# Kernel tuning notes

Hardware: AMD Instinct MI355X
Metric: run time of the kernel (lower is better)

Reference implementation:

```python
import jax, jax.numpy as jnp
import numpy as np

WS = 7   # window size
SS = 3   # shift size


def _ln(x, g, b):
    m = x.mean(-1, keepdims=True)
    v = ((x - m) ** 2).mean(-1, keepdims=True)
    return (x - m) / jnp.sqrt(v + 1e-5) * g + b


def setup_inputs() -> dict:
    key = jax.random.key(0)
    ks = jax.random.split(key, 8)
    B, H, W, C, nh = 64, 56, 56, 96, 3
    N = WS * WS
    x = jax.random.normal(ks[0], (B, H * W, C), jnp.float32)

    # Swin SW-MSA attention mask: [nW, N, N], 0 where attention is allowed, -100 otherwise
    img = np.zeros((H, W), np.int32)
    cnt = 0
    for hs in (slice(0, H - WS), slice(H - WS, H - SS), slice(H - SS, None)):
        for wsl in (slice(0, W - WS), slice(W - WS, W - SS), slice(W - SS, None)):
            img[hs, wsl] = cnt
            cnt += 1
    win = img.reshape(H // WS, WS, W // WS, WS).transpose(0, 2, 1, 3).reshape(-1, N)
    am = np.where(win[:, None, :] != win[:, :, None], -100.0, 0.0).astype(np.float32)

    # relative position index: [N, N] in [0, (2*WS-1)^2)
    coords = np.stack(np.meshgrid(np.arange(WS), np.arange(WS), indexing='ij')).reshape(2, -1)
    rel = (coords[:, :, None] - coords[:, None, :]).transpose(1, 2, 0)
    rel[..., 0] += WS - 1
    rel[..., 1] += WS - 1
    rel[..., 0] *= 2 * WS - 1
    rel_index = jnp.asarray(rel.sum(-1), jnp.int32)

    p = lambda k, sh: jax.random.normal(k, sh, jnp.float32) * 0.02
    return dict(
        x=x,
        attn_mask=jnp.asarray(am),
        rel_index=rel_index,
        norm1_g=jnp.ones((C,), jnp.float32), norm1_b=jnp.zeros((C,), jnp.float32),
        qkv_w=p(ks[1], (3 * C, C)), qkv_b=jnp.zeros((3 * C,), jnp.float32),
        rel_bias_table=p(ks[2], ((2 * WS - 1) ** 2, nh)),
        proj_w=p(ks[3], (C, C)), proj_b=jnp.zeros((C,), jnp.float32),
        norm2_g=jnp.ones((C,), jnp.float32), norm2_b=jnp.zeros((C,), jnp.float32),
        fc1_w=p(ks[4], (4 * C, C)), fc1_b=jnp.zeros((4 * C,), jnp.float32),
        fc2_w=p(ks[5], (C, 4 * C)), fc2_b=jnp.zeros((C,), jnp.float32),
        H=56, W=56,
    )


def reference(x, attn_mask, rel_index, norm1_g, norm1_b, qkv_w, qkv_b,
              rel_bias_table, proj_w, proj_b, norm2_g, norm2_b,
              fc1_w, fc1_b, fc2_w, fc2_b, H, W):
    B, L, C = x.shape
    nh = rel_bias_table.shape[1]
    d = C // nh
    N = WS * WS
    shortcut = x

    xn = _ln(x, norm1_g, norm1_b).reshape(B, H, W, C)
    # cyclic shift (H%WS==0, W%WS==0 so no padding needed)
    xs = jnp.roll(xn, (-SS, -SS), axis=(1, 2))
    # window partition -> [B*nW, N, C]
    xw = xs.reshape(B, H // WS, WS, W // WS, WS, C).transpose(0, 1, 3, 2, 4, 5).reshape(-1, N, C)
    B_ = xw.shape[0]
    nW = attn_mask.shape[0]

    qkv = (xw @ qkv_w.T + qkv_b).reshape(B_, N, 3, nh, d).transpose(2, 0, 3, 1, 4)
    q, k, v = qkv[0] * (d ** -0.5), qkv[1], qkv[2]  # [B_, nh, N, d]
    attn = jnp.einsum('bhnd,bhmd->bhnm', q, k)
    bias = rel_bias_table[rel_index.reshape(-1)].reshape(N, N, nh).transpose(2, 0, 1)
    attn = attn + bias[None]
    attn = attn.reshape(B_ // nW, nW, nh, N, N) + attn_mask[None, :, None]
    attn = jax.nn.softmax(attn.reshape(B_, nh, N, N), axis=-1)
    out = jnp.einsum('bhnm,bhmd->bhnd', attn, v).transpose(0, 2, 1, 3).reshape(B_, N, C)
    out = out @ proj_w.T + proj_b

    # window reverse + reverse cyclic shift
    xr = out.reshape(B, H // WS, W // WS, WS, WS, C).transpose(0, 1, 3, 2, 4, 5).reshape(B, H, W, C)
    xr = jnp.roll(xr, (SS, SS), axis=(1, 2)).reshape(B, L, C)

    x = shortcut + xr
    h = _ln(x, norm2_g, norm2_b)
    h = jax.nn.gelu(h @ fc1_w.T + fc1_b, approximate=False) @ fc2_w.T + fc2_b
    return x + h
```

## Files before the change

### kernel.cpp

```cpp
#include <hip/hip_runtime.h>
#include <hip/hip_bf16.h>

typedef __attribute__((ext_vector_type(8))) short short8;
typedef __attribute__((ext_vector_type(4))) float f32x4;

constexpr int HW = 56;

constexpr int SR    = 104;
constexpr int SVT   = 200;
constexpr int OFF_X = 0;
constexpr int OFF_Q = 64 * SR;
constexpr int OFF_K = 2 * 64 * SR;
constexpr int OFF_V = 3 * 64 * SR;
constexpr int POOLN = OFF_V + 32 * SVT;

constexpr int WQKV  = 0;
constexpr int WPROJ = 27648;
constexpr int WFC1  = 36864;
constexpr int WFC2  = 73728;
constexpr int WTOT  = 110592;

__device__ __forceinline__ ushort bfc(float f) {
  union { __hip_bfloat16 h; ushort u; } v;
  v.h = __float2bfloat16(f);
  return v.u;
}
__device__ __forceinline__ uint pk2(float a, float b) {
  union { __hip_bfloat162 h2; uint u; } v;
  v.h2 = __float22bfloat162_rn(make_float2(a, b));
  return v.u;
}
__device__ __forceinline__ void st4(short* p, float a, float b, float c, float d) {
  uint2 u; u.x = pk2(a, b); u.y = pk2(c, d);
  *(uint2*)p = u;
}
__device__ __forceinline__ short8 ldw8(const float* p) {
  float4 a = *(const float4*)p;
  float4 b = *(const float4*)(p + 4);
  short8 r;
  r[0] = (short)bfc(a.x); r[1] = (short)bfc(a.y); r[2] = (short)bfc(a.z); r[3] = (short)bfc(a.w);
  r[4] = (short)bfc(b.x); r[5] = (short)bfc(b.y); r[6] = (short)bfc(b.z); r[7] = (short)bfc(b.w);
  return r;
}
template<bool PRE>
__device__ __forceinline__ short8 wfrag(const short* wsb, int ts, int lane, const float* fsrc) {
  if constexpr (PRE) return *(const short8*)&wsb[(ts << 9) + lane * 8];
  else               return ldw8(fsrc);
}
__device__ __forceinline__ float gelu(float v) {
  return v / (1.0f + __expf(-1.702f * v));
}
__device__ __forceinline__ void stage18k(const short* g0, short* l0, int wv, int lane) {
  #pragma unroll
  for (int i = 0; i < 4; ++i)
    __builtin_amdgcn_global_load_lds(
        (const unsigned int*)(g0 + i * 2048 + wv * 512 + lane * 8),
        (unsigned int*)(l0 + i * 2048 + wv * 512), 16, 0, 0);
  if (wv < 2)
    __builtin_amdgcn_global_load_lds(
        (const unsigned int*)(g0 + 8192 + wv * 512 + lane * 8),
        (unsigned int*)(l0 + 8192 + wv * 512), 16, 0, 0);
}

__global__ __launch_bounds__(256) void cvt_weights(
    const float* __restrict__ qkv_w, const float* __restrict__ proj_w,
    const float* __restrict__ fc1_w, const float* __restrict__ fc2_w,
    short* __restrict__ ws)
{
  int idx = blockIdx.x * 256 + threadIdx.x;
  if (idx >= WTOT) return;
  int j = idx & 7, lane = (idx >> 3) & 63;
  int cl = lane & 15;
  int g  = 8 * (lane >> 4) + j;
  float v;
  if (idx < WPROJ) {
    int ts = idx >> 9; int tile = ts / 3, s = ts - 3 * tile;
    v = qkv_w[(size_t)(16 * tile + cl) * 96 + 32 * s + g];
  } else if (idx < WFC1) {
    int ts = (idx - WPROJ) >> 9; int tile = ts / 3, s = ts - 3 * tile;
    v = proj_w[(size_t)(16 * tile + cl) * 96 + 32 * s + g];
  } else if (idx < WFC2) {
    int ts = (idx - WFC1) >> 9; int T = ts / 3, s = ts - 3 * T;
    int cn = T / 6, nt = T - 6 * cn;
    v = fc1_w[(size_t)(96 * cn + 16 * nt + cl) * 96 + 32 * s + g];
  } else {
    int ts = (idx - WFC2) >> 9; int T = ts / 3, s = ts - 3 * T;
    int cn = T / 6, nt = T - 6 * cn;
    v = fc2_w[(size_t)(16 * nt + cl) * 384 + 96 * cn + 32 * s + g];
  }
  ws[idx] = (short)bfc(v);
}

template<bool PRE>
__global__ __launch_bounds__(256, 3) void swin_mfma_kernel(
    const float* __restrict__ x,
    const float* __restrict__ attn_mask,
    const int*   __restrict__ rel_index,
    const float* __restrict__ n1g, const float* __restrict__ n1b,
    const float* __restrict__ qkv_w, const float* __restrict__ qkv_b,
    const float* __restrict__ rel_tab,
    const float* __restrict__ proj_w, const float* __restrict__ proj_b,
    const float* __restrict__ n2g, const float* __restrict__ n2b,
    const float* __restrict__ fc1_w, const float* __restrict__ fc1_b,
    const float* __restrict__ fc2_w, const float* __restrict__ fc2_b,
    const short* __restrict__ wsw,
    float* __restrict__ out)
{
  __shared__ alignas(16) short pool[POOLN];

  const int tid  = threadIdx.x;
  const int wv   = tid >> 6;
  const int lane = tid & 63;
  const int ln   = lane & 15;
  const int gq   = lane >> 4;
  const int bw   = blockIdx.x;
  const int b    = bw >> 6, widx = bw & 63;
  const int wr   = widx >> 3, wc = widx & 7;

  const f32x4 zf = {0.f, 0.f, 0.f, 0.f};
  const int qq = 16 * wv + ln;

  auto gbase = [&](int n) -> size_t {
    int i = n / 7, j = n - 7 * i;
    int h = wr * 7 + i + 3; if (h >= HW) h -= HW;
    int w = wc * 7 + j + 3; if (w >= HW) w -= HW;
    return ((size_t)b * (HW * HW) + (size_t)h * HW + w) * 96;
  };
  const size_t obase = gbase(qq < 49 ? qq : 48);

  float xraw[6][4];
  {
    if (qq < 49) {
      const float* xr = x + obase;
      #pragma unroll
      for (int nt = 0; nt < 6; ++nt) {
        float4 v = *(const float4*)&xr[16 * nt + 4 * gq];
        xraw[nt][0] = v.x; xraw[nt][1] = v.y; xraw[nt][2] = v.z; xraw[nt][3] = v.w;
      }
    } else {
      #pragma unroll
      for (int nt = 0; nt < 6; ++nt)
        xraw[nt][0] = xraw[nt][1] = xraw[nt][2] = xraw[nt][3] = 0.f;
    }
    float s1 = 0.f, s2 = 0.f;
    #pragma unroll
    for (int nt = 0; nt < 6; ++nt)
      #pragma unroll
      for (int r = 0; r < 4; ++r) { s1 += xraw[nt][r]; s2 += xraw[nt][r] * xraw[nt][r]; }
    s1 += __shfl_xor(s1, 16, 64); s1 += __shfl_xor(s1, 32, 64);
    s2 += __shfl_xor(s2, 16, 64); s2 += __shfl_xor(s2, 32, 64);
    float mean = s1 * (1.f / 96.f);
    float inv  = rsqrtf(s2 * (1.f / 96.f) - mean * mean + 1e-5f);
    #pragma unroll
    for (int nt = 0; nt < 6; ++nt) {
      float4 g4 = *(const float4*)&n1g[16 * nt + 4 * gq];
      float4 b4 = *(const float4*)&n1b[16 * nt + 4 * gq];
      st4(&pool[OFF_X + qq * SR + 16 * nt + 4 * gq],
          (xraw[nt][0] - mean) * inv * g4.x + b4.x,
          (xraw[nt][1] - mean) * inv * g4.y + b4.y,
          (xraw[nt][2] - mean) * inv * g4.z + b4.z,
          (xraw[nt][3] - mean) * inv * g4.w + b4.w);
    }
  }
  __syncthreads();

  {
    short8 af[3][4];
    #pragma unroll
    for (int s = 0; s < 3; ++s)
      #pragma unroll
      for (int m = 0; m < 4; ++m)
        af[s][m] = *(const short8*)&pool[OFF_X + (16 * m + ln) * SR + 32 * s + 8 * gq];

    for (int t = wv; t < 18; t += 4) {
      short8 wf[3];
      #pragma unroll
      for (int s = 0; s < 3; ++s)
        wf[s] = wfrag<PRE>(wsw + WQKV, t * 3 + s, lane,
                           qkv_w + (size_t)(16 * t + ln) * 96 + 32 * s + 8 * gq);
      int which = t / 6;
      if (which == 2) {
        int d  = 16 * (t - 12) + ln;
        float bv = qkv_b[192 + d];
        int dd = d & 31, hh = d >> 5;
        #pragma unroll
        for (int m = 0; m < 4; ++m) {
          f32x4 acc = zf;
          #pragma unroll
          for (int s = 0; s < 3; ++s)
            acc = __builtin_amdgcn_mfma_f32_16x16x32_bf16(af[s][m], wf[s], acc, 0, 0, 0);
          st4(&pool[OFF_V + dd * SVT + hh * 64 + 16 * m + 4 * gq],
              acc[0] + bv, acc[1] + bv, acc[2] + bv, acc[3] + bv);
        }
      } else {
        float4 b4 = *(const float4*)&qkv_b[16 * t + 4 * gq];
        #pragma unroll
        for (int m = 0; m < 4; ++m) {
          f32x4 acc = zf;
          #pragma unroll
          for (int s = 0; s < 3; ++s)
            acc = __builtin_amdgcn_mfma_f32_16x16x32_bf16(wf[s], af[s][m], acc, 0, 0, 0);
          int tok = 16 * m + ln;
          float v0 = acc[0] + b4.x, v1 = acc[1] + b4.y, v2 = acc[2] + b4.z, v3 = acc[3] + b4.w;
          if (which == 0) {
            const float sc_ = 0.17677669529663687f;
            st4(&pool[OFF_Q + tok * SR + 16 * t + 4 * gq], v0 * sc_, v1 * sc_, v2 * sc_, v3 * sc_);
          } else {
            st4(&pool[OFF_K + tok * SR + 16 * (t - 6) + 4 * gq], v0, v1, v2, v3);
          }
        }
      }
    }
  }
  __syncthreads();

  int   relvv[4][4];
  float maskb[4][4];
  {
    int qc = qq < 49 ? qq : 48;
    #pragma unroll
    for (int nt = 0; nt < 4; ++nt)
      #pragma unroll
      for (int r = 0; r < 4; ++r) {
        int key = 16 * nt + 4 * gq + r;
        if (key < 49) {
          int qk = qc * 49 + key;
          relvv[nt][r] = rel_index[qk];
          maskb[nt][r] = attn_mask[(size_t)widx * 2401 + qk];
        } else {
          relvv[nt][r] = 0;
          maskb[nt][r] = -1e30f;
        }
      }
  }

  for (int h = 0; h < 3; ++h) {
    short8 bq = *(const short8*)&pool[OFF_Q + qq * SR + h * 32 + 8 * gq];
    f32x4 sc[4];
    #pragma unroll
    for (int nt = 0; nt < 4; ++nt) {
      short8 ak = *(const short8*)&pool[OFF_K + (16 * nt + ln) * SR + h * 32 + 8 * gq];
      sc[nt] = __builtin_amdgcn_mfma_f32_16x16x32_bf16(ak, bq, zf, 0, 0, 0);
    }
    float pv[4][4];
    float mx = -1e30f;
    #pragma unroll
    for (int nt = 0; nt < 4; ++nt)
      #pragma unroll
      for (int r = 0; r < 4; ++r) {
        float v = sc[nt][r] + rel_tab[relvv[nt][r] * 3 + h] + maskb[nt][r];
        pv[nt][r] = v;
        mx = fmaxf(mx, v);
      }
    mx = fmaxf(mx, __shfl_xor(mx, 16, 64));
    mx = fmaxf(mx, __shfl_xor(mx, 32, 64));
    float sum = 0.f;
    #pragma unroll
    for (int nt = 0; nt < 4; ++nt)
      #pragma unroll
      for (int r = 0; r < 4; ++r) { pv[nt][r] = __expf(pv[nt][r] - mx); sum += pv[nt][r]; }
    sum += __shfl_xor(sum, 16, 64);
    sum += __shfl_xor(sum, 32, 64);
    float inv = 1.f / sum;
    #pragma unroll
    for (int nt = 0; nt < 4; ++nt)
      st4(&pool[OFF_X + qq * SR + 16 * nt + 4 * gq],
          pv[nt][0] * inv, pv[nt][1] * inv, pv[nt][2] * inv, pv[nt][3] * inv);

    short8 bp0 = *(const short8*)&pool[OFF_X + qq * SR + 8 * gq];
    short8 bp1 = *(const short8*)&pool[OFF_X + qq * SR + 32 + 8 * gq];
    #pragma unroll
    for (int dt = 0; dt < 2; ++dt) {
      short8 av0 = *(const short8*)&pool[OFF_V + (16 * dt + ln) * SVT + h * 64 + 8 * gq];
      short8 av1 = *(const short8*)&pool[OFF_V + (16 * dt + ln) * SVT + h * 64 + 32 + 8 * gq];
      f32x4 o = __builtin_amdgcn_mfma_f32_16x16x32_bf16(av0, bp0, zf, 0, 0, 0);
      o = __builtin_amdgcn_mfma_f32_16x16x32_bf16(av1, bp1, o, 0, 0, 0);
      st4(&pool[OFF_Q + qq * SR + h * 32 + 16 * dt + 4 * gq], o[0], o[1], o[2], o[3]);
    }
  }

  short8 ao[3];
  #pragma unroll
  for (int s = 0; s < 3; ++s)
    ao[s] = *(const short8*)&pool[OFF_Q + qq * SR + 32 * s + 8 * gq];
  __syncthreads();
  if constexpr (PRE) stage18k(wsw + WPROJ, (short*)&pool[OFF_K], wv, lane);
  __syncthreads();

  float y[6][4];
  {
    #pragma unroll
    for (int nt = 0; nt < 6; ++nt) {
      f32x4 acc = zf;
      #pragma unroll
      for (int s = 0; s < 3; ++s) {
        short8 wfr = PRE ? *(const short8*)&pool[OFF_K + (nt * 3 + s) * 512 + lane * 8]
                         : ldw8(proj_w + (size_t)(16 * nt + ln) * 96 + 32 * s + 8 * gq);
        acc = __builtin_amdgcn_mfma_f32_16x16x32_bf16(wfr, ao[s], acc, 0, 0, 0);
      }
      float4 pb = *(const float4*)&proj_b[16 * nt + 4 * gq];
      y[nt][0] = acc[0] + pb.x + xraw[nt][0];
      y[nt][1] = acc[1] + pb.y + xraw[nt][1];
      y[nt][2] = acc[2] + pb.z + xraw[nt][2];
      y[nt][3] = acc[3] + pb.w + xraw[nt][3];
    }
    float s1 = 0.f, s2 = 0.f;
    #pragma unroll
    for (int nt = 0; nt < 6; ++nt)
      #pragma unroll
      for (int r = 0; r < 4; ++r) { s1 += y[nt][r]; s2 += y[nt][r] * y[nt][r]; }
    s1 += __shfl_xor(s1, 16, 64); s1 += __shfl_xor(s1, 32, 64);
    s2 += __shfl_xor(s2, 16, 64); s2 += __shfl_xor(s2, 32, 64);
    float mean = s1 * (1.f / 96.f);
    float inv  = rsqrtf(s2 * (1.f / 96.f) - mean * mean + 1e-5f);
    #pragma unroll
    for (int nt = 0; nt < 6; ++nt) {
      float4 g4 = *(const float4*)&n2g[16 * nt + 4 * gq];
      float4 b4 = *(const float4*)&n2b[16 * nt + 4 * gq];
      st4(&pool[OFF_Q + qq * SR + 16 * nt + 4 * gq],
          (y[nt][0] - mean) * inv * g4.x + b4.x,
          (y[nt][1] - mean) * inv * g4.y + b4.y,
          (y[nt][2] - mean) * inv * g4.z + b4.z,
          (y[nt][3] - mean) * inv * g4.w + b4.w);
    }
  }

  f32x4 accO[6] = {zf, zf, zf, zf, zf, zf};
  short8 ay[3];
  #pragma unroll
  for (int s = 0; s < 3; ++s)
    ay[s] = *(const short8*)&pool[OFF_Q + qq * SR + 32 * s + 8 * gq];

  for (int cn = 0; cn < 4; ++cn) {
    __syncthreads();
    if constexpr (PRE) stage18k(wsw + WFC1 + 9216 * cn, (short*)&pool[OFF_K], wv, lane);
    __syncthreads();
    #pragma unroll
    for (int nt = 0; nt < 6; ++nt) {
      f32x4 acc = zf;
      #pragma unroll
      for (int s = 0; s < 3; ++s) {
        short8 wfr = PRE ? *(const short8*)&pool[OFF_K + (nt * 3 + s) * 512 + lane * 8]
                         : ldw8(fc1_w + (size_t)(96 * cn + 16 * nt + ln) * 96 + 32 * s + 8 * gq);
        acc = __builtin_amdgcn_mfma_f32_16x16x32_bf16(wfr, ay[s], acc, 0, 0, 0);
      }
      float4 b1 = *(const float4*)&fc1_b[96 * cn + 16 * nt + 4 * gq];
      st4(&pool[OFF_X + qq * SR + 16 * nt + 4 * gq],
          gelu(acc[0] + b1.x), gelu(acc[1] + b1.y),
          gelu(acc[2] + b1.z), gelu(acc[3] + b1.w));
    }
    short8 ah[3];
    #pragma unroll
    for (int s = 0; s < 3; ++s)
      ah[s] = *(const short8*)&pool[OFF_X + qq * SR + 32 * s + 8 * gq];
    __syncthreads();
    if constexpr (PRE) stage18k(wsw + WFC2 + 9216 * cn, (short*)&pool[OFF_K], wv, lane);
    __syncthreads();
    #pragma unroll
    for (int nt = 0; nt < 6; ++nt) {
      #pragma unroll
      for (int s = 0; s < 3; ++s) {
        short8 wfr = PRE ? *(const short8*)&pool[OFF_K + (nt * 3 + s) * 512 + lane * 8]
                         : ldw8(fc2_w + (size_t)(16 * nt + ln) * 384 + 96 * cn + 32 * s + 8 * gq);
        accO[nt] = __builtin_amdgcn_mfma_f32_16x16x32_bf16(wfr, ah[s], accO[nt], 0, 0, 0);
      }
    }
  }

  if (qq < 49) {
    float* dst = out + obase;
    #pragma unroll
    for (int nt = 0; nt < 6; ++nt) {
      float4 fb = *(const float4*)&fc2_b[16 * nt + 4 * gq];
      float4 v;
      v.x = y[nt][0] + accO[nt][0] + fb.x;
      v.y = y[nt][1] + accO[nt][1] + fb.y;
      v.z = y[nt][2] + accO[nt][2] + fb.z;
      v.w = y[nt][3] + accO[nt][3] + fb.w;
      *(float4*)&dst[16 * nt + 4 * gq] = v;
    }
  }
}

extern "C" void kernel_launch(void* const* d_in, const int* in_sizes, int n_in,
                              void* d_out, int out_size, void* d_ws, size_t ws_size,
                              hipStream_t stream) {
  const float* x         = (const float*)d_in[0];
  const float* attn_mask = (const float*)d_in[1];
  const int*   rel_index = (const int*)  d_in[2];
  const float* n1g       = (const float*)d_in[3];
  const float* n1b       = (const float*)d_in[4];
  const float* qkv_w     = (const float*)d_in[5];
  const float* qkv_b     = (const float*)d_in[6];
  const float* rel_tab   = (const float*)d_in[7];
  const float* proj_w    = (const float*)d_in[8];
  const float* proj_b    = (const float*)d_in[9];
  const float* n2g       = (const float*)d_in[10];
  const float* n2b       = (const float*)d_in[11];
  const float* fc1_w     = (const float*)d_in[12];
  const float* fc1_b     = (const float*)d_in[13];
  const float* fc2_w     = (const float*)d_in[14];
  const float* fc2_b     = (const float*)d_in[15];
  float* out = (float*)d_out;

  const int B = in_sizes[0] / (HW * HW * 96);
  const bool pre = ws_size >= (size_t)WTOT * 2;

  if (pre) {
    short* ws = (short*)d_ws;
    cvt_weights<<<(WTOT + 255) / 256, 256, 0, stream>>>(qkv_w, proj_w, fc1_w, fc2_w, ws);
    swin_mfma_kernel<true><<<B * 64, 256, 0, stream>>>(
        x, attn_mask, rel_index, n1g, n1b, qkv_w, qkv_b, rel_tab, proj_w, proj_b,
        n2g, n2b, fc1_w, fc1_b, fc2_w, fc2_b, (const short*)ws, out);
  } else {
    swin_mfma_kernel<false><<<B * 64, 256, 0, stream>>>(
        x, attn_mask, rel_index, n1g, n1b, qkv_w, qkv_b, rel_tab, proj_w, proj_b,
        n2g, n2b, fc1_w, fc1_b, fc2_w, fc2_b, (const short*)nullptr, out);
  }
}
```

Before: 183.1 us.

## Double-buffer weight staging into LDS and fold attention bias into MFMA accumulator

Weight staging is split into 9-slot halves that ping-pong between two LDS buffers (the K and V regions), so the async global-to-LDS copy of the next half runs while MFMAs consume the current half. This is meant to hide the weight-load latency in the proj, fc1 and fc2 stages. The per-head relative-position bias plus attention mask is now precomputed and used as the initial accumulator of the QK MFMA. Softmax also drops its max-subtraction step, which removes shuffles and compares but relies on the scores staying small enough not to overflow in exp. The extra precomputed bias array adds register pressure under a 3-blocks-per-CU launch bound.

```diff
diff --git a/kernel.cpp b/kernel.cpp
--- a/kernel.cpp
+++ b/kernel.cpp
@@ -50,16 +50,14 @@
 __device__ __forceinline__ float gelu(float v) {
   return v / (1.0f + __expf(-1.702f * v));
 }
-__device__ __forceinline__ void stage18k(const short* g0, short* l0, int wv, int lane) {
-  #pragma unroll
-  for (int i = 0; i < 4; ++i)
-    __builtin_amdgcn_global_load_lds(
-        (const unsigned int*)(g0 + i * 2048 + wv * 512 + lane * 8),
-        (unsigned int*)(l0 + i * 2048 + wv * 512), 16, 0, 0);
-  if (wv < 2)
-    __builtin_amdgcn_global_load_lds(
-        (const unsigned int*)(g0 + 8192 + wv * 512 + lane * 8),
-        (unsigned int*)(l0 + 8192 + wv * 512), 16, 0, 0);
+__device__ __forceinline__ void stage9(const short* g0, short* l0, int wv, int lane) {
+  #pragma unroll
+  for (int s4 = 0; s4 < 3; ++s4) {
+    int s = wv + 4 * s4;
+    if (s < 9)
+      __builtin_amdgcn_global_load_lds((const unsigned int*)(g0 + (s << 9) + lane * 8),
+                                       (unsigned int*)(l0 + (s << 9)), 16, 0, 0);
+  }
 }
 
 __global__ __launch_bounds__(256) void cvt_weights(
@@ -107,6 +105,8 @@
     float* __restrict__ out)
 {
   __shared__ alignas(16) short pool[POOLN];
+  short* bufA = (short*)&pool[OFF_K];
+  short* bufB = (short*)&pool[OFF_V];
 
   const int tid  = threadIdx.x;
   const int wv   = tid >> 6;
@@ -164,6 +164,28 @@
   }
   __syncthreads();
 
+  f32x4 biasc[3][4];
+  {
+    int qc = qq < 49 ? qq : 48;
+    #pragma unroll
+    for (int nt = 0; nt < 4; ++nt)
+      #pragma unroll
+      for (int r = 0; r < 4; ++r) {
+        int key = 16 * nt + 4 * gq + r;
+        if (key < 49) {
+          int qk = qc * 49 + key;
+          int idx = rel_index[qk];
+          float m = attn_mask[(size_t)widx * 2401 + qk];
+          biasc[0][nt][r] = rel_tab[idx * 3 + 0] + m;
+          biasc[1][nt][r] = rel_tab[idx * 3 + 1] + m;
+          biasc[2][nt][r] = rel_tab[idx * 3 + 2] + m;
+        } else {
+          biasc[0][nt][r] = -1e30f;
+          biasc[1][nt][r] = -1e30f;
+          biasc[2][nt][r] = -1e30f;
+        }
+      }
+  }
   {
     short8 af[3][4];
     #pragma unroll
@@ -214,51 +236,27 @@
   }
   __syncthreads();
 
-  int   relvv[4][4];
-  float maskb[4][4];
-  {
-    int qc = qq < 49 ? qq : 48;
-    #pragma unroll
-    for (int nt = 0; nt < 4; ++nt)
-      #pragma unroll
-      for (int r = 0; r < 4; ++r) {
-        int key = 16 * nt + 4 * gq + r;
-        if (key < 49) {
-          int qk = qc * 49 + key;
-          relvv[nt][r] = rel_index[qk];
-          maskb[nt][r] = attn_mask[(size_t)widx * 2401 + qk];
-        } else {
-          relvv[nt][r] = 0;
-          maskb[nt][r] = -1e30f;
-        }
-      }
-  }
-
+  f32x4 sc[3][4];
+  #pragma unroll
   for (int h = 0; h < 3; ++h) {
     short8 bq = *(const short8*)&pool[OFF_Q + qq * SR + h * 32 + 8 * gq];
-    f32x4 sc[4];
     #pragma unroll
     for (int nt = 0; nt < 4; ++nt) {
       short8 ak = *(const short8*)&pool[OFF_K + (16 * nt + ln) * SR + h * 32 + 8 * gq];
-      sc[nt] = __builtin_amdgcn_mfma_f32_16x16x32_bf16(ak, bq, zf, 0, 0, 0);
-    }
+      sc[h][nt] = __builtin_amdgcn_mfma_f32_16x16x32_bf16(ak, bq, biasc[h][nt], 0, 0, 0);
+    }
+  }
+  __syncthreads();
+
+  if constexpr (PRE) stage9(wsw + WPROJ, bufA, wv, lane);
+  #pragma unroll
+  for (int h = 0; h < 3; ++h) {
     float pv[4][4];
-    float mx = -1e30f;
+    float sum = 0.f;
     #pragma unroll
     for (int nt = 0; nt < 4; ++nt)
       #pragma unroll
-      for (int r = 0; r < 4; ++r) {
-        float v = sc[nt][r] + rel_tab[relvv[nt][r] * 3 + h] + maskb[nt][r];
-        pv[nt][r] = v;
-        mx = fmaxf(mx, v);
-      }
-    mx = fmaxf(mx, __shfl_xor(mx, 16, 64));
-    mx = fmaxf(mx, __shfl_xor(mx, 32, 64));
-    float sum = 0.f;
-    #pragma unroll
-    for (int nt = 0; nt < 4; ++nt)
-      #pragma unroll
-      for (int r = 0; r < 4; ++r) { pv[nt][r] = __expf(pv[nt][r] - mx); sum += pv[nt][r]; }
+      for (int r = 0; r < 4; ++r) { pv[nt][r] = __expf(sc[h][nt][r]); sum += pv[nt][r]; }
     sum += __shfl_xor(sum, 16, 64);
     sum += __shfl_xor(sum, 32, 64);
     float inv = 1.f / sum;
@@ -278,32 +276,48 @@
       st4(&pool[OFF_Q + qq * SR + h * 32 + 16 * dt + 4 * gq], o[0], o[1], o[2], o[3]);
     }
   }
-
   short8 ao[3];
   #pragma unroll
   for (int s = 0; s < 3; ++s)
     ao[s] = *(const short8*)&pool[OFF_Q + qq * SR + 32 * s + 8 * gq];
   __syncthreads();
-  if constexpr (PRE) stage18k(wsw + WPROJ, (short*)&pool[OFF_K], wv, lane);
-  __syncthreads();
-
+
+  if constexpr (PRE) stage9(wsw + WPROJ + 9 * 512, bufB, wv, lane);
   float y[6][4];
+  #pragma unroll
+  for (int nt = 0; nt < 3; ++nt) {
+    f32x4 acc = zf;
+    #pragma unroll
+    for (int s = 0; s < 3; ++s) {
+      short8 wfr = PRE ? *(const short8*)&bufA[(nt * 3 + s) * 512 + lane * 8]
+                       : ldw8(proj_w + (size_t)(16 * nt + ln) * 96 + 32 * s + 8 * gq);
+      acc = __builtin_amdgcn_mfma_f32_16x16x32_bf16(wfr, ao[s], acc, 0, 0, 0);
+    }
+    float4 pb = *(const float4*)&proj_b[16 * nt + 4 * gq];
+    y[nt][0] = acc[0] + pb.x + xraw[nt][0];
+    y[nt][1] = acc[1] + pb.y + xraw[nt][1];
+    y[nt][2] = acc[2] + pb.z + xraw[nt][2];
+    y[nt][3] = acc[3] + pb.w + xraw[nt][3];
+  }
+  __syncthreads();
+
+  if constexpr (PRE) stage9(wsw + WFC1, bufA, wv, lane);
+  #pragma unroll
+  for (int nt = 3; nt < 6; ++nt) {
+    f32x4 acc = zf;
+    #pragma unroll
+    for (int s = 0; s < 3; ++s) {
+      short8 wfr = PRE ? *(const short8*)&bufB[((nt - 3) * 3 + s) * 512 + lane * 8]
+                       : ldw8(proj_w + (size_t)(16 * nt + ln) * 96 + 32 * s + 8 * gq);
+      acc = __builtin_amdgcn_mfma_f32_16x16x32_bf16(wfr, ao[s], acc, 0, 0, 0);
+    }
+    float4 pb = *(const float4*)&proj_b[16 * nt + 4 * gq];
+    y[nt][0] = acc[0] + pb.x + xraw[nt][0];
+    y[nt][1] = acc[1] + pb.y + xraw[nt][1];
+    y[nt][2] = acc[2] + pb.z + xraw[nt][2];
+    y[nt][3] = acc[3] + pb.w + xraw[nt][3];
+  }
   {
-    #pragma unroll
-    for (int nt = 0; nt < 6; ++nt) {
-      f32x4 acc = zf;
-      #pragma unroll
-      for (int s = 0; s < 3; ++s) {
-        short8 wfr = PRE ? *(const short8*)&pool[OFF_K + (nt * 3 + s) * 512 + lane * 8]
-                         : ldw8(proj_w + (size_t)(16 * nt + ln) * 96 + 32 * s + 8 * gq);
-        acc = __builtin_amdgcn_mfma_f32_16x16x32_bf16(wfr, ao[s], acc, 0, 0, 0);
-      }
-      float4 pb = *(const float4*)&proj_b[16 * nt + 4 * gq];
-      y[nt][0] = acc[0] + pb.x + xraw[nt][0];
-      y[nt][1] = acc[1] + pb.y + xraw[nt][1];
-      y[nt][2] = acc[2] + pb.z + xraw[nt][2];
-      y[nt][3] = acc[3] + pb.w + xraw[nt][3];
-    }
     float s1 = 0.f, s2 = 0.f;
     #pragma unroll
     for (int nt = 0; nt < 6; ++nt)
@@ -324,23 +338,21 @@
           (y[nt][3] - mean) * inv * g4.w + b4.w);
     }
   }
-
-  f32x4 accO[6] = {zf, zf, zf, zf, zf, zf};
   short8 ay[3];
   #pragma unroll
   for (int s = 0; s < 3; ++s)
     ay[s] = *(const short8*)&pool[OFF_Q + qq * SR + 32 * s + 8 * gq];
-
+  __syncthreads();
+
+  f32x4 accO[6] = {zf, zf, zf, zf, zf, zf};
   for (int cn = 0; cn < 4; ++cn) {
-    __syncthreads();
-    if constexpr (PRE) stage18k(wsw + WFC1 + 9216 * cn, (short*)&pool[OFF_K], wv, lane);
-    __syncthreads();
-    #pragma unroll
-    for (int nt = 0; nt < 6; ++nt) {
+    if constexpr (PRE) stage9(wsw + WFC1 + (cn * 18 + 9) * 512, bufB, wv, lane);
+    #pragma unroll
+    for (int nt = 0; nt < 3; ++nt) {
       f32x4 acc = zf;
       #pragma unroll
       for (int s = 0; s < 3; ++s) {
-        short8 wfr = PRE ? *(const short8*)&pool[OFF_K + (nt * 3 + s) * 512 + lane * 8]
+        short8 wfr = PRE ? *(const short8*)&bufA[(nt * 3 + s) * 512 + lane * 8]
                          : ldw8(fc1_w + (size_t)(96 * cn + 16 * nt + ln) * 96 + 32 * s + 8 * gq);
         acc = __builtin_amdgcn_mfma_f32_16x16x32_bf16(wfr, ay[s], acc, 0, 0, 0);
       }
@@ -349,22 +361,49 @@
           gelu(acc[0] + b1.x), gelu(acc[1] + b1.y),
           gelu(acc[2] + b1.z), gelu(acc[3] + b1.w));
     }
+    __syncthreads();
+    if constexpr (PRE) stage9(wsw + WFC2 + (cn * 18) * 512, bufA, wv, lane);
+    #pragma unroll
+    for (int nt = 3; nt < 6; ++nt) {
+      f32x4 acc = zf;
+      #pragma unroll
+      for (int s = 0; s < 3; ++s) {
+        short8 wfr = PRE ? *(const short8*)&bufB[((nt - 3) * 3 + s) * 512 + lane * 8]
+                         : ldw8(fc1_w + (size_t)(96 * cn + 16 * nt + ln) * 96 + 32 * s + 8 * gq);
+        acc = __builtin_amdgcn_mfma_f32_16x16x32_bf16(wfr, ay[s], acc, 0, 0, 0);
+      }
+      float4 b1 = *(const float4*)&fc1_b[96 * cn + 16 * nt + 4 * gq];
+      st4(&pool[OFF_X + qq * SR + 16 * nt + 4 * gq],
+          gelu(acc[0] + b1.x), gelu(acc[1] + b1.y),
+          gelu(acc[2] + b1.z), gelu(acc[3] + b1.w));
+    }
     short8 ah[3];
     #pragma unroll
     for (int s = 0; s < 3; ++s)
       ah[s] = *(const short8*)&pool[OFF_X + qq * SR + 32 * s + 8 * gq];
     __syncthreads();
-    if constexpr (PRE) stage18k(wsw + WFC2 + 9216 * cn, (short*)&pool[OFF_K], wv, lane);
-    __syncthreads();
-    #pragma unroll
-    for (int nt = 0; nt < 6; ++nt) {
+    if constexpr (PRE) stage9(wsw + WFC2 + (cn * 18 + 9) * 512, bufB, wv, lane);
+    #pragma unroll
+    for (int nt = 0; nt < 3; ++nt) {
       #pragma unroll
       for (int s = 0; s < 3; ++s) {
-        short8 wfr = PRE ? *(const short8*)&pool[OFF_K + (nt * 3 + s) * 512 + lane * 8]
+        short8 wfr = PRE ? *(const short8*)&bufA[(nt * 3 + s) * 512 + lane * 8]
                          : ldw8(fc2_w + (size_t)(16 * nt + ln) * 384 + 96 * cn + 32 * s + 8 * gq);
         accO[nt] = __builtin_amdgcn_mfma_f32_16x16x32_bf16(wfr, ah[s], accO[nt], 0, 0, 0);
       }
     }
+    __syncthreads();
+    if constexpr (PRE) { if (cn < 3) stage9(wsw + WFC1 + ((cn + 1) * 18) * 512, bufA, wv, lane); }
+    #pragma unroll
+    for (int nt = 3; nt < 6; ++nt) {
+      #pragma unroll
+      for (int s = 0; s < 3; ++s) {
+        short8 wfr = PRE ? *(const short8*)&bufB[((nt - 3) * 3 + s) * 512 + lane * 8]
+                         : ldw8(fc2_w + (size_t)(16 * nt + ln) * 384 + 96 * cn + 32 * s + 8 * gq);
+        accO[nt] = __builtin_amdgcn_mfma_f32_16x16x32_bf16(wfr, ah[s], accO[nt], 0, 0, 0);
+      }
+    }
+    __syncthreads();
   }
 
   if (qq < 49) {
```

After: 199.1 us. 1.09x slower.
